# Kernel tuning notes

Measured on AMD Instinct MI355X. Metric: run time of the kernel, lower is better.

Reference implementation:

```python
import jax, jax.numpy as jnp
import numpy as np

UP = 2          # upsample factor used by upfirdn2d.upsample2d default
FILTER = [1, 2, 1]


def _make_fir_kernel():
    # CreateLowpassKernel: convolve([1,2,1],[1,1]) -> [1,3,3,1]; outer product; normalize.
    k1 = np.convolve(np.asarray(FILTER, np.float32), [1.0, 1.0]).reshape(1, -1)
    k = k1.T @ k1
    k = k / k.sum()
    # upsample2d applies gain = up**2
    return jnp.asarray(k * (UP ** 2), dtype=jnp.float32)  # [4,4]


def setup_inputs() -> dict:
    key = jax.random.key(0)
    kx, kw = jax.random.split(key)
    B, Cin, Cout, H, W = 16, 512, 512, 64, 64
    x = jax.random.normal(kx, (B, Cin, H, W), dtype=jnp.float32)
    fir_kernel = _make_fir_kernel()
    # MSR init for 1x1 conv: std = 1/sqrt(in_ch * k*k) = 1/sqrt(Cin)
    w = jax.random.normal(kw, (Cout, Cin, 1, 1), dtype=jnp.float32) / np.sqrt(Cin)
    b = jnp.zeros((Cout,), dtype=jnp.float32)
    return {"x": x, "fir_kernel": fir_kernel, "w": w, "b": b}


def _upsample2d(x, fir_kernel):
    # upfirdn2d: zero-insert by UP, pad ((fw+UP-1)//2, (fw-UP)//2) = (2,1), convolve with flipped FIR.
    C = x.shape[1]
    fw = fir_kernel.shape[-1]
    k = fir_kernel[::-1, ::-1]                       # flip -> true convolution
    dw = jnp.broadcast_to(k, (C, 1, fw, fw))         # depthwise kernel [C,1,4,4]
    pad = ((fw + UP - 1) // 2, (fw - UP) // 2)       # (2, 1)
    return jax.lax.conv_general_dilated(
        x, dw,
        window_strides=(1, 1),
        padding=(pad, pad),
        lhs_dilation=(UP, UP),                       # zero-insertion upsample
        dimension_numbers=("NCHW", "OIHW", "NCHW"),
        feature_group_count=C,
    )


def reference(x, fir_kernel, w, b):
    y = _upsample2d(x, fir_kernel)                   # [B,C,2H,2W]
    # Convolution.forward nan/inf guard (no-op for finite inputs)
    y = jnp.nan_to_num(y, nan=0.0, posinf=1.0, neginf=-1.0)
    # 1x1 conv projection + bias
    out = jnp.einsum("bchw,oc->bohw", y, w[:, :, 0, 0]) + b[None, :, None, None]
    return out
```

## Files before the change

kernel.cpp:

```cpp
#include <hip/hip_runtime.h>


#define B_   16
#define CIN  512
#define COUT 512
#define S_   4096
#define HO   127
#define WO   127

typedef unsigned int  u32;
typedef unsigned short u16;
typedef __attribute__((ext_vector_type(8))) short  bf16x8;
typedef __attribute__((ext_vector_type(8))) u16    u16x8;
typedef __attribute__((ext_vector_type(4))) float  f32x4;

static __device__ __forceinline__ u16 f2bf(float f) {
  u32 u = __float_as_uint(f);
  u += 0x7FFFu + ((u >> 16) & 1u);
  return (u16)(u >> 16);
}
static __device__ __forceinline__ float bf2f(u16 h) {
  return __uint_as_float(((u32)h) << 16);
}

#if defined(__has_builtin)
#if __has_builtin(__builtin_amdgcn_global_load_lds)
#define HAS_GLOAD 1
#endif
#endif
#ifndef HAS_GLOAD
#define HAS_GLOAD 0
#endif

#if HAS_GLOAD
static __device__ __forceinline__ void gload16(const char* g, char* l) {
  __builtin_amdgcn_global_load_lds(
      (const __attribute__((address_space(1))) unsigned int*)g,
      (__attribute__((address_space(3))) unsigned int*)l, 16, 0, 0);
}
#endif


__global__ __launch_bounds__(256) void conv_w_kernel(
    const float* __restrict__ w, u16* __restrict__ wt) {
  int g = blockIdx.x * 256 + threadIdx.x;
  int t_idx = g >> 9;
  int u = g & 511;
  int to = t_idx >> 4, tk = t_idx & 15;
  int r = u & 127, kg = u >> 7;
  int o = to * 128 + r;
  int c = tk * 32 + kg * 8;
  const float4* src = reinterpret_cast<const float4*>(w + (size_t)o * CIN + c);
  float4 lo = src[0], hi = src[1];
  u16x8 pk;
  pk[0] = f2bf(lo.x); pk[1] = f2bf(lo.y); pk[2] = f2bf(lo.z); pk[3] = f2bf(lo.w);
  pk[4] = f2bf(hi.x); pk[5] = f2bf(hi.y); pk[6] = f2bf(hi.z); pk[7] = f2bf(hi.w);
  *reinterpret_cast<u16x8*>(wt + (size_t)g * 8) = pk;
}

__global__ __launch_bounds__(256) void conv_x_kernel(
    const float* __restrict__ x, u16* __restrict__ xt) {
  int ts = blockIdx.x, tk = blockIdx.y, b = blockIdx.z;
  int t = threadIdx.x;
  __shared__ float lf[32 * 128];
  const float* src = x + ((size_t)(b * CIN + tk * 32)) * S_ + ts * 128;
#pragma unroll
  for (int i = 0; i < 4; ++i) {
    int q = i * 256 + t;
    int c = q >> 5, sq = q & 31;
    *reinterpret_cast<float4*>(&lf[c * 128 + sq * 4]) =
        *reinterpret_cast<const float4*>(src + (size_t)c * S_ + sq * 4);
  }
  __syncthreads();
  size_t tile_base = (((size_t)(b * 32 + ts)) * 16 + tk) * 512;
#pragma unroll
  for (int i = 0; i < 2; ++i) {
    int u = i * 256 + t;
    int kg = u >> 7, r = u & 127;
    u16x8 pk;
#pragma unroll
    for (int e = 0; e < 8; ++e) pk[e] = f2bf(lf[(kg * 8 + e) * 128 + r]);
    *reinterpret_cast<u16x8*>(xt + (tile_base + u) * 8) = pk;
  }
}

__global__ __launch_bounds__(256) void gemm_kernel(
    const u16* __restrict__ wt, const u16* __restrict__ xt,
    u16* __restrict__ z) {
  int nt = blockIdx.x, mt = blockIdx.y, b = blockIdx.z;
  int t = threadIdx.x;
  __shared__ short lds[8192];
  char* lA = (char*)&lds[0];
  char* lB = lA + 8192;

  int lane = t & 63, wid = t >> 6;
  int wr = wid >> 1, wc = wid & 1;
  int lr = lane & 15, kg = lane >> 4;

  f32x4 acc[4][4];
#pragma unroll
  for (int m = 0; m < 4; ++m)
#pragma unroll
    for (int n = 0; n < 4; ++n) acc[m][n] = f32x4{0.f, 0.f, 0.f, 0.f};

  const char* gA = (const char*)wt + (size_t)(mt * 16) * 8192;
  const char* gB = (const char*)xt + ((size_t)(b * 32 + nt)) * 16 * 8192;

  int abyte[4], bbyte[4];
#pragma unroll
  for (int m = 0; m < 4; ++m) abyte[m] = (kg * 128 + wr * 64 + m * 16 + lr) * 16;
#pragma unroll
  for (int n = 0; n < 4; ++n) bbyte[n] = (kg * 128 + wc * 64 + n * 16 + lr) * 16;

  for (int ks = 0; ks < 16; ++ks) {
    const char* pA = gA + (size_t)ks * 8192;
    const char* pB = gB + (size_t)ks * 8192;
#if HAS_GLOAD
    __syncthreads();
    gload16(pA + t * 16, lA + t * 16);
    gload16(pA + 4096 + t * 16, lA + 4096 + t * 16);
    gload16(pB + t * 16, lB + t * 16);
    gload16(pB + 4096 + t * 16, lB + 4096 + t * 16);
    __syncthreads();
#else
    u16x8 va0 = *reinterpret_cast<const u16x8*>(pA + t * 16);
    u16x8 va1 = *reinterpret_cast<const u16x8*>(pA + 4096 + t * 16);
    u16x8 vb0 = *reinterpret_cast<const u16x8*>(pB + t * 16);
    u16x8 vb1 = *reinterpret_cast<const u16x8*>(pB + 4096 + t * 16);
    __syncthreads();
    *reinterpret_cast<u16x8*>(lA + t * 16) = va0;
    *reinterpret_cast<u16x8*>(lA + 4096 + t * 16) = va1;
    *reinterpret_cast<u16x8*>(lB + t * 16) = vb0;
    *reinterpret_cast<u16x8*>(lB + 4096 + t * 16) = vb1;
    __syncthreads();
#endif
    bf16x8 av[4], bv[4];
#pragma unroll
    for (int m = 0; m < 4; ++m)
      av[m] = *reinterpret_cast<const bf16x8*>(lA + abyte[m]);
#pragma unroll
    for (int n = 0; n < 4; ++n)
      bv[n] = *reinterpret_cast<const bf16x8*>(lB + bbyte[n]);
#pragma unroll
    for (int m = 0; m < 4; ++m)
#pragma unroll
      for (int n = 0; n < 4; ++n)
        acc[m][n] = __builtin_amdgcn_mfma_f32_16x16x32_bf16(
            av[m], bv[n], acc[m][n], 0, 0, 0);
  }

  int o_b = mt * 128 + wr * 64 + kg * 4;
  int s_b = nt * 128 + wc * 64 + lr;
#pragma unroll
  for (int m = 0; m < 4; ++m)
#pragma unroll
    for (int n = 0; n < 4; ++n) {
      f32x4 v = acc[m][n];
      size_t base = ((size_t)(b * COUT + o_b + m * 16)) * S_ + (s_b + n * 16);
#pragma unroll
      for (int r = 0; r < 4; ++r) z[base + (size_t)r * S_] = f2bf(v[r]);
    }
}

__global__ __launch_bounds__(256) void upsample_kernel(
    const u16* __restrict__ z, const float* __restrict__ bias,
    float* __restrict__ out) {
  int t = threadIdx.x;
  int lane = t & 63;
  int bo = blockIdx.x * 4 + (t >> 6);
  const u16* zp = z + ((size_t)bo << 12) + lane;
  float bv = bias[bo & 511];
  float* ob = out + (size_t)bo * (HO * WO) + 2 * lane;

  float wl = (lane == 0) ? 0.f : 1.f;
  bool has_j1 = (lane < 63);

  u16 c_ = zp[0], l_ = zp[-1], r_ = zp[1];
  float hA_p = 0.f, hB_p = 0.f;

  for (int m = 0; m < 64; ++m) {
    float zc = bf2f(c_), zl = bf2f(l_) * wl, zr = bf2f(r_);
    if (m < 63) {
      const u16* q = zp + 64;
      c_ = q[0]; l_ = q[-1]; r_ = q[1];
      zp = q;
    }
    float hA = fmaf(3.f, zc, zl);
    float hB = fmaf(3.f, zc, zr);

    float* p_even = ob + (u32)(2 * m) * WO;
    if (m > 0) {
      float* p_odd = p_even - WO;
      p_odd[0] = fmaf(fmaf(3.f, hA_p, hA), 0.0625f, bv);
      if (has_j1) p_odd[1] = fmaf(fmaf(3.f, hB_p, hB), 0.0625f, bv);
    }
    p_even[0] = fmaf(fmaf(3.f, hA, hA_p), 0.0625f, bv);
    if (has_j1) p_even[1] = fmaf(fmaf(3.f, hB, hB_p), 0.0625f, bv);

    hA_p = hA; hB_p = hB;
  }
}

__global__ __launch_bounds__(256) void fallback_kernel(
    const float* __restrict__ x, const float* __restrict__ w,
    const float* __restrict__ bias, float* __restrict__ out) {
  u32 idx = blockIdx.x * 256u + threadIdx.x;
  const u32 total = (u32)B_ * COUT * HO * WO;
  if (idx >= total) return;
  u32 j = idx % WO;
  u32 r1 = idx / WO;
  u32 i = r1 % HO;
  u32 bo = r1 / HO;
  int o = (int)(bo & 511u);
  int b = (int)(bo >> 9);
  int m = (int)(i >> 1), n = (int)(j >> 1);
  int ie = !(i & 1), je = !(j & 1);
  int rA = ie ? m - 1 : m;
  int cA = je ? n - 1 : n;
  float w_r0 = ie ? 1.f : 3.f, w_r1 = ie ? 3.f : 1.f;
  float w_c0 = je ? 1.f : 3.f, w_c1 = je ? 3.f : 1.f;
  const float* xb = x + (size_t)b * CIN * S_;
  float acc = 0.f;
  for (int c = 0; c < CIN; ++c) {
    const float* xc = xb + (size_t)c * S_;
    float y = 0.f;
    if (rA >= 0) {
      if (cA >= 0) y += w_r0 * w_c0 * xc[rA * 64 + cA];
      y += w_r0 * w_c1 * xc[rA * 64 + cA + 1];
    }
    if (cA >= 0) y += w_r1 * w_c0 * xc[(rA + 1) * 64 + cA];
    y += w_r1 * w_c1 * xc[(rA + 1) * 64 + cA + 1];
    acc += y * w[(size_t)o * CIN + c];
  }
  out[idx] = acc * 0.0625f + bias[o];
}

extern "C" void kernel_launch(void* const* d_in, const int* in_sizes, int n_in,
                              void* d_out, int out_size, void* d_ws,
                              size_t ws_size, hipStream_t stream) {
  const float* x = (const float*)d_in[0];
  const float* w = (const float*)d_in[2];
  const float* bias = (const float*)d_in[3];
  float* out = (float*)d_out;

  const size_t xt_bytes = (size_t)B_ * S_ * CIN * 2;
  const size_t wt_off = xt_bytes;
  const size_t wt_bytes = (size_t)COUT * CIN * 2;
  const size_t z_off = wt_off + ((wt_bytes + 255) & ~(size_t)255);
  const size_t need = z_off + (size_t)B_ * COUT * S_ * 2;
  const size_t total_out = (size_t)B_ * COUT * HO * WO;
  const u32 nblk_out = (u32)((total_out + 255) / 256);

  if (ws_size >= need) {
    u16* xt = (u16*)d_ws;
    u16* wt = (u16*)((char*)d_ws + wt_off);
    u16* zz = (u16*)((char*)d_ws + z_off);
    conv_w_kernel<<<128, 256, 0, stream>>>(w, wt);
    conv_x_kernel<<<dim3(32, 16, B_), 256, 0, stream>>>(x, xt);
    gemm_kernel<<<dim3(32, 4, B_), 256, 0, stream>>>(wt, xt, zz);
    upsample_kernel<<<(B_ * COUT) / 4, 256, 0, stream>>>(zz, bias, out);
  } else {
    fallback_kernel<<<nblk_out, 256, 0, stream>>>(x, w, bias, out);
  }
}
```

Before: 281.5 us.

## Fuse 1x1-conv GEMM with FIR upsample epilogue, dropping intermediate z buffer

Replaces the separate GEMM and upsample kernels with one fused kernel. Each block keeps a 32-output-channel weight slice resident in LDS, walks spatial row tiles, stages GEMM results in LDS, and applies the 4x4 FIR upsample plus bias directly to the output. This removes the bf16 intermediate z round trip through global memory and one launch, and keeps z in fp32. In exchange the grid is only 512 blocks using about 74KB of LDS each, tiles are small (2x2 MFMA per wave), and the halo tile is recomputed at each split boundary.

```diff
diff --git a/kernel.cpp b/kernel.cpp
--- a/kernel.cpp
+++ b/kernel.cpp
@@ -18,9 +18,6 @@
   u32 u = __float_as_uint(f);
   u += 0x7FFFu + ((u >> 16) & 1u);
   return (u16)(u >> 16);
-}
-static __device__ __forceinline__ float bf2f(u16 h) {
-  return __uint_as_float(((u32)h) << 16);
 }
 
 #if defined(__has_builtin)
@@ -84,120 +81,166 @@
   }
 }
 
-__global__ __launch_bounds__(256) void gemm_kernel(
+#define WL_OFF 0
+#define BL_OFF 32768
+#define ZL_OFF 49152
+#define CL_OFF 65792
+#define SMEM_BYTES 74112
+
+__global__ __launch_bounds__(256) void fused_kernel(
     const u16* __restrict__ wt, const u16* __restrict__ xt,
-    u16* __restrict__ z) {
-  int nt = blockIdx.x, mt = blockIdx.y, b = blockIdx.z;
+    const float* __restrict__ bias, float* __restrict__ out) {
+  extern __shared__ char smem[];
+  char* Wl = smem + WL_OFF;
+  char* Bl = smem + BL_OFF;
+  float* zl = (float*)(smem + ZL_OFF);
+  float* cl = (float*)(smem + CL_OFF);
+
   int t = threadIdx.x;
-  __shared__ short lds[8192];
-  char* lA = (char*)&lds[0];
-  char* lB = lA + 8192;
-
-  int lane = t & 63, wid = t >> 6;
-  int wr = wid >> 1, wc = wid & 1;
+  int sh = blockIdx.x, op = blockIdx.y, b = blockIdx.z;
+  int lane = t & 63, wv = t >> 6;
   int lr = lane & 15, kg = lane >> 4;
-
-  f32x4 acc[4][4];
-#pragma unroll
-  for (int m = 0; m < 4; ++m)
-#pragma unroll
-    for (int n = 0; n < 4; ++n) acc[m][n] = f32x4{0.f, 0.f, 0.f, 0.f};
-
-  const char* gA = (const char*)wt + (size_t)(mt * 16) * 8192;
-  const char* gB = (const char*)xt + ((size_t)(b * 32 + nt)) * 16 * 8192;
-
-  int abyte[4], bbyte[4];
-#pragma unroll
-  for (int m = 0; m < 4; ++m) abyte[m] = (kg * 128 + wr * 64 + m * 16 + lr) * 16;
-#pragma unroll
-  for (int n = 0; n < 4; ++n) bbyte[n] = (kg * 128 + wc * 64 + n * 16 + lr) * 16;
-
-  for (int ks = 0; ks < 16; ++ks) {
-    const char* pA = gA + (size_t)ks * 8192;
-    const char* pB = gB + (size_t)ks * 8192;
+  int to = op >> 2, opq = op & 3;
+
 #if HAS_GLOAD
+#pragma unroll
+  for (int u = 0; u < 8; ++u) {
+    int L = u * 256 + t;
+    int tk = L >> 7, kq = (L >> 5) & 3, r = L & 31;
+    size_t gu = ((size_t)(to * 16 + tk)) * 512 + (size_t)(kq * 128 + opq * 32 + r);
+    gload16((const char*)wt + gu * 16, Wl + (size_t)L * 16);
+  }
+#else
+  {
+    u16x8 tmp[8];
+#pragma unroll
+    for (int u = 0; u < 8; ++u) {
+      int L = u * 256 + t;
+      int tk = L >> 7, kq = (L >> 5) & 3, r = L & 31;
+      size_t gu = ((size_t)(to * 16 + tk)) * 512 + (size_t)(kq * 128 + opq * 32 + r);
+      tmp[u] = *reinterpret_cast<const u16x8*>((const char*)wt + gu * 16);
+    }
+#pragma unroll
+    for (int u = 0; u < 8; ++u)
+      *reinterpret_cast<u16x8*>(Wl + (size_t)(u * 256 + t) * 16) = tmp[u];
+  }
+#endif
+  for (int i = t; i < 2080; i += 256) cl[i] = 0.f;
+  __syncthreads();
+
+  int uo = t & 31, pr = (t >> 5) & 1, q = t >> 6;
+  int o_glob = op * 32 + uo;
+  float bvv = bias[o_glob];
+  float* obase = out + ((size_t)b * 512 + o_glob) * (size_t)(HO * WO);
+
+  int st0 = sh * 16;
+  for (int ts = st0 - (sh ? 1 : 0); ts < st0 + 16; ++ts) {
+    bool wout = (ts >= st0);
+
+    f32x4 acc[2][2];
+#pragma unroll
+    for (int m = 0; m < 2; ++m)
+#pragma unroll
+      for (int n = 0; n < 2; ++n) acc[m][n] = f32x4{0.f, 0.f, 0.f, 0.f};
+
+    const char* xb = (const char*)xt + ((size_t)(b * 32 + ts) * 16) * 8192;
+    for (int k2 = 0; k2 < 8; ++k2) {
+      const char* px = xb + (size_t)k2 * 16384;
+      __syncthreads();
+#if HAS_GLOAD
+#pragma unroll
+      for (int qq = 0; qq < 4; ++qq)
+        gload16(px + qq * 4096 + t * 16, Bl + qq * 4096 + t * 16);
+      __syncthreads();
+#else
+      {
+        u16x8 tb[4];
+#pragma unroll
+        for (int qq = 0; qq < 4; ++qq)
+          tb[qq] = *reinterpret_cast<const u16x8*>(px + qq * 4096 + t * 16);
+        __syncthreads();
+#pragma unroll
+        for (int qq = 0; qq < 4; ++qq)
+          *reinterpret_cast<u16x8*>(Bl + qq * 4096 + t * 16) = tb[qq];
+        __syncthreads();
+      }
+#endif
+#pragma unroll
+      for (int kk = 0; kk < 2; ++kk) {
+        int ks = k2 * 2 + kk;
+        bf16x8 av[2], bw[2];
+#pragma unroll
+        for (int m = 0; m < 2; ++m)
+          av[m] = *reinterpret_cast<const bf16x8*>(
+              Wl + ks * 2048 + (kg * 32 + m * 16 + lr) * 16);
+#pragma unroll
+        for (int n = 0; n < 2; ++n)
+          bw[n] = *reinterpret_cast<const bf16x8*>(
+              Bl + kk * 8192 + (kg * 128 + wv * 32 + n * 16 + lr) * 16);
+#pragma unroll
+        for (int m = 0; m < 2; ++m)
+#pragma unroll
+          for (int n = 0; n < 2; ++n)
+            acc[m][n] = __builtin_amdgcn_mfma_f32_16x16x32_bf16(
+                av[m], bw[n], acc[m][n], 0, 0, 0);
+      }
+    }
+
     __syncthreads();
-    gload16(pA + t * 16, lA + t * 16);
-    gload16(pA + 4096 + t * 16, lA + 4096 + t * 16);
-    gload16(pB + t * 16, lB + t * 16);
-    gload16(pB + 4096 + t * 16, lB + 4096 + t * 16);
+#pragma unroll
+    for (int m = 0; m < 2; ++m)
+#pragma unroll
+      for (int n = 0; n < 2; ++n) {
+        int s_loc = wv * 32 + n * 16 + lr;
+        float* zp = zl + (s_loc >> 6) * 2080 + (s_loc & 63);
+#pragma unroll
+        for (int r = 0; r < 4; ++r) {
+          int o_loc = m * 16 + kg * 4 + r;
+          zp[o_loc * 65] = acc[m][n][r];
+        }
+      }
     __syncthreads();
-#else
-    u16x8 va0 = *reinterpret_cast<const u16x8*>(pA + t * 16);
-    u16x8 va1 = *reinterpret_cast<const u16x8*>(pA + 4096 + t * 16);
-    u16x8 vb0 = *reinterpret_cast<const u16x8*>(pB + t * 16);
-    u16x8 vb1 = *reinterpret_cast<const u16x8*>(pB + 4096 + t * 16);
+
+    const float* pA = pr ? (zl + uo * 65) : (cl + uo * 65);
+    const float* pB = pr ? (zl + 2080 + uo * 65) : (zl + uo * 65);
+    int nlo = q * 16 - 1;
+    float zA[18], zB[18];
+    zA[0] = (q == 0) ? 0.f : pA[nlo];
+    zB[0] = (q == 0) ? 0.f : pB[nlo];
+#pragma unroll
+    for (int i = 1; i < 18; ++i) { zA[i] = pA[nlo + i]; zB[i] = pB[nlo + i]; }
+
+    int r0 = 4 * ts - 1 + 2 * pr;
+    float* p0 = obase + (size_t)r0 * WO + q * 32;
+    float* p1 = p0 + WO;
+#pragma unroll
+    for (int ch = 0; ch < 8; ++ch) {
+      float v0[4], v1[4];
+#pragma unroll
+      for (int e = 0; e < 4; ++e) {
+        int jj = ch * 4 + e;
+        int ln = (jj + 1) >> 1;
+        float tA = (jj & 1) ? 3.f : 1.f;
+        float tB = (jj & 1) ? 1.f : 3.f;
+        if (q == 0 && jj == 0) tA = 0.f;
+        float gA = tA * zA[ln] + tB * zA[ln + 1];
+        float gB = tA * zB[ln] + tB * zB[ln + 1];
+        v0[e] = fmaf(fmaf(3.f, gA, gB), 0.0625f, bvv);
+        v1[e] = fmaf(fmaf(3.f, gB, gA), 0.0625f, bvv);
+      }
+      if (wout) {
+        bool tail = (q == 3) && (ch == 7);
+        if (!tail) {
+          if (r0 >= 0) __builtin_memcpy(p0 + ch * 4, v0, 16);
+          __builtin_memcpy(p1 + ch * 4, v1, 16);
+        } else {
+          if (r0 >= 0) { p0[28] = v0[0]; p0[29] = v0[1]; p0[30] = v0[2]; }
+          p1[28] = v1[0]; p1[29] = v1[1]; p1[30] = v1[2];
+        }
+      }
+    }
     __syncthreads();
-    *reinterpret_cast<u16x8*>(lA + t * 16) = va0;
-    *reinterpret_cast<u16x8*>(lA + 4096 + t * 16) = va1;
-    *reinterpret_cast<u16x8*>(lB + t * 16) = vb0;
-    *reinterpret_cast<u16x8*>(lB + 4096 + t * 16) = vb1;
-    __syncthreads();
-#endif
-    bf16x8 av[4], bv[4];
-#pragma unroll
-    for (int m = 0; m < 4; ++m)
-      av[m] = *reinterpret_cast<const bf16x8*>(lA + abyte[m]);
-#pragma unroll
-    for (int n = 0; n < 4; ++n)
-      bv[n] = *reinterpret_cast<const bf16x8*>(lB + bbyte[n]);
-#pragma unroll
-    for (int m = 0; m < 4; ++m)
-#pragma unroll
-      for (int n = 0; n < 4; ++n)
-        acc[m][n] = __builtin_amdgcn_mfma_f32_16x16x32_bf16(
-            av[m], bv[n], acc[m][n], 0, 0, 0);
-  }
-
-  int o_b = mt * 128 + wr * 64 + kg * 4;
-  int s_b = nt * 128 + wc * 64 + lr;
-#pragma unroll
-  for (int m = 0; m < 4; ++m)
-#pragma unroll
-    for (int n = 0; n < 4; ++n) {
-      f32x4 v = acc[m][n];
-      size_t base = ((size_t)(b * COUT + o_b + m * 16)) * S_ + (s_b + n * 16);
-#pragma unroll
-      for (int r = 0; r < 4; ++r) z[base + (size_t)r * S_] = f2bf(v[r]);
-    }
-}
-
-__global__ __launch_bounds__(256) void upsample_kernel(
-    const u16* __restrict__ z, const float* __restrict__ bias,
-    float* __restrict__ out) {
-  int t = threadIdx.x;
-  int lane = t & 63;
-  int bo = blockIdx.x * 4 + (t >> 6);
-  const u16* zp = z + ((size_t)bo << 12) + lane;
-  float bv = bias[bo & 511];
-  float* ob = out + (size_t)bo * (HO * WO) + 2 * lane;
-
-  float wl = (lane == 0) ? 0.f : 1.f;
-  bool has_j1 = (lane < 63);
-
-  u16 c_ = zp[0], l_ = zp[-1], r_ = zp[1];
-  float hA_p = 0.f, hB_p = 0.f;
-
-  for (int m = 0; m < 64; ++m) {
-    float zc = bf2f(c_), zl = bf2f(l_) * wl, zr = bf2f(r_);
-    if (m < 63) {
-      const u16* q = zp + 64;
-      c_ = q[0]; l_ = q[-1]; r_ = q[1];
-      zp = q;
-    }
-    float hA = fmaf(3.f, zc, zl);
-    float hB = fmaf(3.f, zc, zr);
-
-    float* p_even = ob + (u32)(2 * m) * WO;
-    if (m > 0) {
-      float* p_odd = p_even - WO;
-      p_odd[0] = fmaf(fmaf(3.f, hA_p, hA), 0.0625f, bv);
-      if (has_j1) p_odd[1] = fmaf(fmaf(3.f, hB_p, hB), 0.0625f, bv);
-    }
-    p_even[0] = fmaf(fmaf(3.f, hA, hA_p), 0.0625f, bv);
-    if (has_j1) p_even[1] = fmaf(fmaf(3.f, hB, hB_p), 0.0625f, bv);
-
-    hA_p = hA; hB_p = hB;
+    for (int i = t; i < 2080; i += 256) cl[i] = zl[2080 + i];
   }
 }
 
@@ -246,19 +289,16 @@
   const size_t xt_bytes = (size_t)B_ * S_ * CIN * 2;
   const size_t wt_off = xt_bytes;
   const size_t wt_bytes = (size_t)COUT * CIN * 2;
-  const size_t z_off = wt_off + ((wt_bytes + 255) & ~(size_t)255);
-  const size_t need = z_off + (size_t)B_ * COUT * S_ * 2;
+  const size_t need = wt_off + wt_bytes;
   const size_t total_out = (size_t)B_ * COUT * HO * WO;
   const u32 nblk_out = (u32)((total_out + 255) / 256);
 
   if (ws_size >= need) {
     u16* xt = (u16*)d_ws;
     u16* wt = (u16*)((char*)d_ws + wt_off);
-    u16* zz = (u16*)((char*)d_ws + z_off);
     conv_w_kernel<<<128, 256, 0, stream>>>(w, wt);
     conv_x_kernel<<<dim3(32, 16, B_), 256, 0, stream>>>(x, xt);
-    gemm_kernel<<<dim3(32, 4, B_), 256, 0, stream>>>(wt, xt, zz);
-    upsample_kernel<<<(B_ * COUT) / 4, 256, 0, stream>>>(zz, bias, out);
+    fused_kernel<<<dim3(2, 16, B_), 256, SMEM_BYTES, stream>>>(wt, xt, bias, out);
   } else {
     fallback_kernel<<<nblk_out, 256, 0, stream>>>(x, w, bias, out);
   }
```

Result: slower. 441.5 us (+56.9%).

## Stage upsample input plane in LDS and write 8 outputs per thread vectorized

Applied to the files above, without the earlier changes.

The upsample kernel now gives each output plane its own block. The block stages the 64x64 bf16 tile into shared memory using vectorized 16-byte loads and a padded stride. Each thread then computes 8 consecutive output columns for two output rows and writes them with wide stores. Before, each thread issued scattered scalar stores of two floats and redundant neighbour loads from global memory. The aim is better memory coalescing on the large output write, at the cost of LDS use, a barrier, and odd-width handling at the edge column.

```diff
diff --git a/kernel.cpp b/kernel.cpp
--- a/kernel.cpp
+++ b/kernel.cpp
@@ -162,42 +162,75 @@
     }
 }
 
+#define ZSTRIDE 66
 __global__ __launch_bounds__(256) void upsample_kernel(
     const u16* __restrict__ z, const float* __restrict__ bias,
     float* __restrict__ out) {
+  int bo = blockIdx.x;
   int t = threadIdx.x;
-  int lane = t & 63;
-  int bo = blockIdx.x * 4 + (t >> 6);
-  const u16* zp = z + ((size_t)bo << 12) + lane;
+  __shared__ u16 zl[64 * ZSTRIDE];
+
+  {
+    const u16x8* src = reinterpret_cast<const u16x8*>(z + ((size_t)bo << 12));
+    u16x8 v0 = src[t];
+    u16x8 v1 = src[t + 256];
+    int r0 = t >> 3, c0 = (t & 7) * 8;
+    int r1 = (t + 256) >> 3, c1 = (t & 7) * 8;
+    u16* p0 = &zl[r0 * ZSTRIDE + c0];
+    u16* p1 = &zl[r1 * ZSTRIDE + c1];
+#pragma unroll
+    for (int e = 0; e < 8; ++e) { p0[e] = (u16)v0[e]; p1[e] = (u16)v1[e]; }
+  }
   float bv = bias[bo & 511];
-  float* ob = out + (size_t)bo * (HO * WO) + 2 * lane;
-
-  float wl = (lane == 0) ? 0.f : 1.f;
-  bool has_j1 = (lane < 63);
-
-  u16 c_ = zp[0], l_ = zp[-1], r_ = zp[1];
-  float hA_p = 0.f, hB_p = 0.f;
-
-  for (int m = 0; m < 64; ++m) {
-    float zc = bf2f(c_), zl = bf2f(l_) * wl, zr = bf2f(r_);
-    if (m < 63) {
-      const u16* q = zp + 64;
-      c_ = q[0]; l_ = q[-1]; r_ = q[1];
-      zp = q;
-    }
-    float hA = fmaf(3.f, zc, zl);
-    float hB = fmaf(3.f, zc, zr);
-
-    float* p_even = ob + (u32)(2 * m) * WO;
-    if (m > 0) {
-      float* p_odd = p_even - WO;
-      p_odd[0] = fmaf(fmaf(3.f, hA_p, hA), 0.0625f, bv);
-      if (has_j1) p_odd[1] = fmaf(fmaf(3.f, hB_p, hB), 0.0625f, bv);
-    }
-    p_even[0] = fmaf(fmaf(3.f, hA, hA_p), 0.0625f, bv);
-    if (has_j1) p_even[1] = fmaf(fmaf(3.f, hB, hB_p), 0.0625f, bv);
-
-    hA_p = hA; hB_p = hB;
+  __syncthreads();
+
+  int c = t & 15;
+  int mr = t >> 4;
+  float* ob = out + (size_t)bo * (HO * WO) + 8 * c;
+  int n0 = 4 * c - 1;
+  int i0 = (c == 0) ? 0 : n0;
+
+  for (int it = 0; it < 4; ++it) {
+    int m = it * 16 + mr;
+    const u16* rA = &zl[((m == 0) ? 0 : (m - 1)) * ZSTRIDE];
+    const u16* rB = &zl[m * ZSTRIDE];
+    float a[6], d[6];
+    a[0] = bf2f(rA[i0]); d[0] = bf2f(rB[i0]);
+#pragma unroll
+    for (int k = 1; k < 6; ++k) {
+      a[k] = bf2f(rA[n0 + k]);
+      d[k] = bf2f(rB[n0 + k]);
+    }
+    float wa = (m == 0) ? 0.f : 1.f;
+
+    float v0[8], v1[8];
+#pragma unroll
+    for (int e = 0; e < 8; ++e) {
+      int li = (e == 0) ? 0 : (1 + ((e - 1) >> 1));
+      float tA = (e & 1) ? 3.f : 1.f;
+      float tB = (e & 1) ? 1.f : 3.f;
+      if (c == 0 && e == 0) tA = 0.f;
+      float gA = wa * (tA * a[li] + tB * a[li + 1]);
+      float gB = tA * d[li] + tB * d[li + 1];
+      v0[e] = fmaf(fmaf(3.f, gA, gB), 0.0625f, bv);
+      v1[e] = fmaf(fmaf(3.f, gB, gA), 0.0625f, bv);
+    }
+
+    float* p1p = ob + (size_t)(2 * m) * WO;
+    float* p0p = p1p - WO;
+    if (c < 15) {
+      if (m > 0) __builtin_memcpy(p0p, v0, 32);
+      __builtin_memcpy(p1p, v1, 32);
+    } else {
+      if (m > 0) {
+        __builtin_memcpy(p0p, v0, 16);
+        __builtin_memcpy(p0p + 4, &v0[4], 8);
+        p0p[6] = v0[6];
+      }
+      __builtin_memcpy(p1p, v1, 16);
+      __builtin_memcpy(p1p + 4, &v1[4], 8);
+      p1p[6] = v1[6];
+    }
   }
 }
 
@@ -221,8 +254,8 @@
   float w_c0 = je ? 1.f : 3.f, w_c1 = je ? 3.f : 1.f;
   const float* xb = x + (size_t)b * CIN * S_;
   float acc = 0.f;
-  for (int c = 0; c < CIN; ++c) {
-    const float* xc = xb + (size_t)c * S_;
+  for (int cc = 0; cc < CIN; ++cc) {
+    const float* xc = xb + (size_t)cc * S_;
     float y = 0.f;
     if (rA >= 0) {
       if (cA >= 0) y += w_r0 * w_c0 * xc[rA * 64 + cA];
@@ -230,7 +263,7 @@
     }
     if (cA >= 0) y += w_r1 * w_c0 * xc[(rA + 1) * 64 + cA];
     y += w_r1 * w_c1 * xc[(rA + 1) * 64 + cA + 1];
-    acc += y * w[(size_t)o * CIN + c];
+    acc += y * w[(size_t)o * CIN + cc];
   }
   out[idx] = acc * 0.0625f + bias[o];
 }
@@ -258,7 +291,7 @@
     conv_w_kernel<<<128, 256, 0, stream>>>(w, wt);
     conv_x_kernel<<<dim3(32, 16, B_), 256, 0, stream>>>(x, xt);
     gemm_kernel<<<dim3(32, 4, B_), 256, 0, stream>>>(wt, xt, zz);
-    upsample_kernel<<<(B_ * COUT) / 4, 256, 0, stream>>>(zz, bias, out);
+    upsample_kernel<<<B_ * COUT, 256, 0, stream>>>(zz, bias, out);
   } else {
     fallback_kernel<<<nblk_out, 256, 0, stream>>>(x, w, bias, out);
   }
```

After: 314.1 us. 1.12x slower.
